# Kernel tuning notes

Hardware: AMD Instinct MI355X
Metric: run time of the kernel (lower is better)

Reference implementation:

```python
import jax, jax.numpy as jnp
import numpy as np

DIM = 1024
DIM_LATENT = 1024
DIM_HEAD = 64
INNER = max(DIM, DIM_LATENT)  # 1024
HEADS = INNER // DIM_HEAD     # 16
SCALE = DIM_HEAD ** -0.5
LN_EPS = 1e-5
RMS_EPS = 1e-8


def layernorm(x, g, b):
    mu = jnp.mean(x, axis=-1, keepdims=True)
    var = jnp.mean(jnp.square(x - mu), axis=-1, keepdims=True)
    return (x - mu) * jax.lax.rsqrt(var + LN_EPS) * g + b


def rmsnorm(x, gamma):
    # torch: x / clamp(norm(x,-1) * d**-0.5, eps) * gamma
    n = jnp.linalg.norm(x, axis=-1, keepdims=True) * (x.shape[-1] ** -0.5)
    return x / jnp.maximum(n, RMS_EPS) * gamma


def setup_inputs() -> dict:
    key = jax.random.key(0)
    ks = jax.random.split(key, 8)
    b, n, nl = 8, 2048, 512
    x = jax.random.normal(ks[0], (b, n, DIM), dtype=jnp.float32)
    latents = jax.random.normal(ks[1], (b, nl, DIM_LATENT), dtype=jnp.float32)
    mask = jax.random.randint(ks[2], (b, n), 0, 2).astype(bool)
    init = lambda k, shape, fan_in: jax.random.normal(k, shape, jnp.float32) * (fan_in ** -0.5)
    return {
        "x": x,
        "latents": latents,
        "mask": mask,
        "ln_x_g": jnp.ones((DIM,), jnp.float32),
        "ln_x_b": jnp.zeros((DIM,), jnp.float32),
        "ln_l_g": jnp.ones((DIM_LATENT,), jnp.float32),
        "ln_l_b": jnp.zeros((DIM_LATENT,), jnp.float32),
        "q_gamma": jnp.ones((DIM_HEAD,), jnp.float32),
        "k_gamma": jnp.ones((DIM_HEAD,), jnp.float32),
        "W_q": init(ks[3], (DIM_LATENT, INNER), DIM_LATENT),
        "W_kv": init(ks[4], (DIM, 2 * INNER), DIM),
        "W_out": init(ks[5], (INNER, DIM_LATENT), INNER),
        "b_out": jnp.zeros((DIM_LATENT,), jnp.float32),
    }


def reference(x, latents, mask, ln_x_g, ln_x_b, ln_l_g, ln_l_b,
              q_gamma, k_gamma, W_q, W_kv, W_out, b_out):
    b, n, _ = x.shape
    nl = latents.shape[1]
    xn = layernorm(x, ln_x_g, ln_x_b)
    ln = layernorm(latents, ln_l_g, ln_l_b)

    q = ln @ W_q                                   # [b, nl, inner]
    kv = jnp.concatenate([xn @ W_kv, ln @ W_kv], axis=1)  # [b, n+nl, 2*inner]
    k, v = kv[..., :INNER], kv[..., INNER:]

    to_heads = lambda t: t.reshape(t.shape[0], t.shape[1], HEADS, DIM_HEAD).transpose(0, 2, 1, 3)
    q, k, v = to_heads(q), to_heads(k), to_heads(v)  # [b, h, *, d]

    qn = rmsnorm(q, q_gamma) * SCALE
    kn = rmsnorm(k, k_gamma)

    sim = jnp.einsum('bhid,bhjd->bhij', qn, kn)      # [b, h, nl, n+nl]
    full_mask = jnp.pad(mask, ((0, 0), (0, nl)), constant_values=True)
    neg = -jnp.finfo(sim.dtype).max
    sim = jnp.where(full_mask[:, None, None, :], sim, neg)

    attn = jax.nn.softmax(sim.astype(jnp.float32), axis=-1).astype(sim.dtype)
    out = jnp.einsum('bhij,bhjd->bhid', attn, v)     # [b, h, nl, d]
    out = out.transpose(0, 2, 1, 3).reshape(b, nl, INNER)
    return out @ W_out + b_out
```

## Files before the change

### kernel.cpp

```cpp
#include <hip/hip_runtime.h>
#include <hip/hip_bf16.h>
#include <cfloat>
#include <cmath>

typedef __hip_bfloat16 bf16;
#define DEV_INLINE __device__ __forceinline__

typedef __attribute__((ext_vector_type(8))) short short8;
typedef __attribute__((ext_vector_type(4))) short short4v;
typedef __attribute__((ext_vector_type(4))) float float4v;
typedef __attribute__((ext_vector_type(16))) float float16v;

#define BATCH 8
#define NSEQ 2048
#define NLAT 512
#define DIM_ 1024
#define NKV 2560
#define HEADS_ 16
#define DHEAD 64
#define SCALE_ 0.125f
#define LN_EPS_ 1e-5f
#define RMS_EPS_ 1e-8f

DEV_INLINE float bf2f(bf16 v) { return __bfloat162float(v); }
DEV_INLINE bf16 f2bf(float v) { return __float2bfloat16(v); }
DEV_INLINE short bfbits(float x) { union { bf16 b; short s; } c; c.b = f2bf(x); return c.s; }
DEV_INLINE float sbits2f(short s) { union { bf16 b; short s; } c; c.s = s; return bf2f(c.b); }

DEV_INLINE int detect_bf16(const void* ones) {
    return (*(const unsigned*)ones == 0x3F803F80u) ? 1 : 0;
}

template<typename T> DEV_INLINE float ldf(const T* p);
template<> DEV_INLINE float ldf<float>(const float* p) { return *p; }
template<> DEV_INLINE float ldf<bf16>(const bf16* p)  { return __bfloat162float(*p); }

DEV_INLINE void gload16(const bf16* g, bf16* l) {
    __builtin_amdgcn_global_load_lds(
        (const __attribute__((address_space(1))) unsigned int*)g,
        (__attribute__((address_space(3))) unsigned int*)l,
        16, 0, 0);
}

DEV_INLINE float block_sum_256(float v, float* sred) {
    #pragma unroll
    for (int o = 1; o < 64; o <<= 1) v += __shfl_xor(v, o, 64);
    int w = threadIdx.x >> 6;
    __syncthreads();
    if ((threadIdx.x & 63) == 0) sred[w] = v;
    __syncthreads();
    return sred[0] + sred[1] + sred[2] + sred[3];
}

template<typename T>
DEV_INLINE void ln_row_body(int r, const void* xv, const void* latv,
                            const void* gxv, const void* bxv,
                            const void* glv, const void* blv,
                            bf16* __restrict__ out, float* sred)
{
    const T* src; const T* g; const T* be; bf16* o;
    if (r < BATCH * NSEQ) {
        int b = r >> 11, i = r & 2047;
        src = (const T*)xv + (size_t)r * DIM_;
        o = out + ((size_t)b * NKV + i) * DIM_;
        g = (const T*)gxv; be = (const T*)bxv;
    } else {
        int rr = r - BATCH * NSEQ;
        int b = rr >> 9, i = rr & 511;
        src = (const T*)latv + (size_t)rr * DIM_;
        o = out + ((size_t)b * NKV + NSEQ + i) * DIM_;
        g = (const T*)glv; be = (const T*)blv;
    }
    int t = threadIdx.x;
    float v[4];
    float s = 0.f;
    #pragma unroll
    for (int j = 0; j < 4; j++) { v[j] = ldf(src + t + j * 256); s += v[j]; }
    s = block_sum_256(s, sred);
    float mu = s * (1.f / 1024.f);
    float s2 = 0.f;
    #pragma unroll
    for (int j = 0; j < 4; j++) { float d = v[j] - mu; s2 += d * d; }
    s2 = block_sum_256(s2, sred);
    float rstd = rsqrtf(s2 * (1.f / 1024.f) + LN_EPS_);
    #pragma unroll
    for (int j = 0; j < 4; j++) {
        int c = t + j * 256;
        o[c] = f2bf((v[j] - mu) * rstd * ldf(g + c) + ldf(be + c));
    }
}

template<typename T>
DEV_INLINE void trans_body(int bid, const void* wqv, const void* wkvv, const void* woutv,
                           bf16* wqT, bf16* wkvT, bf16* woutT, float* tile )
{
    const T* in; bf16* out; int N, t0;
    if (bid < 1024)      { in = (const T*)wqv;   out = wqT;   N = 1024; t0 = bid; }
    else if (bid < 3072) { in = (const T*)wkvv;  out = wkvT;  N = 2048; t0 = bid - 1024; }
    else                 { in = (const T*)woutv; out = woutT; N = 1024; t0 = bid - 3072; }
    int K = 1024;
    int nb = N >> 5;
    int bn = (t0 % nb) * 32, bk = (t0 / nb) * 32;
    int tx = threadIdx.x & 31, ty = threadIdx.x >> 5;
    #pragma unroll
    for (int j = 0; j < 4; j++)
        tile[(ty + j * 8) * 33 + tx] = ldf(in + (size_t)(bk + ty + j * 8) * N + bn + tx);
    __syncthreads();
    #pragma unroll
    for (int j = 0; j < 4; j++)
        out[(size_t)(bn + ty + j * 8) * K + bk + tx] = f2bf(tile[tx * 33 + ty + j * 8]);
}

__global__ __launch_bounds__(256) void prep_kernel(
    const void* x, const void* lat,
    const void* gx, const void* bx, const void* gl, const void* bl,
    const void* wq, const void* wkv, const void* wout,
    bf16* __restrict__ cat_n, bf16* __restrict__ wqT,
    bf16* __restrict__ wkvT, bf16* __restrict__ woutT)
{
    __shared__ float smem[32 * 33];
    int isb = detect_bf16(gx);
    int bid = blockIdx.x;
    if (bid < 20480) {
        if (isb) ln_row_body<bf16>(bid, x, lat, gx, bx, gl, bl, cat_n, smem);
        else     ln_row_body<float>(bid, x, lat, gx, bx, gl, bl, cat_n, smem);
    } else {
        int t = bid - 20480;
        if (isb) trans_body<bf16>(t, wq, wkv, wout, wqT, wkvT, woutT, smem);
        else     trans_body<float>(t, wq, wkv, wout, wqT, wkvT, woutT, smem);
    }
}

#define MFMA_CORE_128(As, Bs, Apt, Bpt, K, acc)                                \
    {                                                                          \
        bf16* Asl_ = &As[threadIdx.x * 8];                                     \
        bf16* Bsl_ = &Bs[threadIdx.x * 8];                                     \
        for (int k0 = 0; k0 < K; k0 += 64) {                                   \
            __syncthreads();                                                   \
            _Pragma("unroll")                                                  \
            for (int rep = 0; rep < 4; rep++) {                                \
                gload16(Apt[rep] + k0, Asl_ + rep * 2048);                     \
                gload16(Bpt[rep] + k0, Bsl_ + rep * 2048);                     \
            }                                                                  \
            __syncthreads();                                                   \
            _Pragma("unroll")                                                  \
            for (int kk = 0; kk < 4; kk++) {                                   \
                short8 af_[2], bf_[2];                                         \
                _Pragma("unroll")                                              \
                for (int ms = 0; ms < 2; ms++) {                               \
                    int row = wm * 64 + ms * 32 + l32;                         \
                    int jc = (kk * 2 + h5) ^ (row & 7);                        \
                    af_[ms] = *(const short8*)&As[row * 64 + jc * 8];          \
                }                                                              \
                _Pragma("unroll")                                              \
                for (int ns = 0; ns < 2; ns++) {                               \
                    int row = wn * 64 + ns * 32 + l32;                         \
                    int jc = (kk * 2 + h5) ^ (row & 7);                        \
                    bf_[ns] = *(const short8*)&Bs[row * 64 + jc * 8];          \
                }                                                              \
                _Pragma("unroll")                                              \
                for (int ms = 0; ms < 2; ms++)                                 \
                    _Pragma("unroll")                                          \
                    for (int ns = 0; ns < 2; ns++)                             \
                        acc[ms][ns] = __builtin_amdgcn_mfma_f32_32x32x16_bf16( \
                            af_[ms], bf_[ns], acc[ms][ns], 0, 0, 0);           \
            }                                                                  \
        }                                                                      \
    }

__global__ __launch_bounds__(256) void gemm_qkv(
    const void* gq, const void* gk,
    const bf16* __restrict__ cat_n, const bf16* __restrict__ wkvT,
    const bf16* __restrict__ wqT,
    bf16* __restrict__ kbuf, bf16* __restrict__ vtbuf, bf16* __restrict__ qbuf)
{
    __shared__ bf16 As[128 * 64];
    __shared__ bf16 Bs[128 * 64];
    int isb = detect_bf16(gq);

    int tid = threadIdx.x;
    int bid = blockIdx.x;
    int wv = tid >> 6, lane = tid & 63, l32 = lane & 31, h5 = lane >> 5;
    int wm = wv >> 1, wn = wv & 1;

    const bf16* Bt; int bn, bm; bool isq;
    if (bid < 2560) {
        bm = (bid >> 7) * 8 + (bid & 7);
        bn = (bid >> 3) & 15;
        Bt = wkvT; isq = false;
    } else {
        int t = bid - 2560;
        bm = (t >> 6) * 8 + (t & 7);
        bn = (t >> 3) & 7;
        Bt = wqT; isq = true;
    }
    const int K = 1024;

    const bf16* Apt[4]; const bf16* Bpt[4];
    #pragma unroll
    for (int rep = 0; rep < 4; rep++) {
        int c = rep * 256 + tid;
        int row = c >> 3;
        int k8 = ((c & 7) ^ (row & 7)) * 8;
        int ar = bm * 128 + row;
        int am = isq ? ((ar >> 9) * NKV + NSEQ + (ar & 511)) : ar;
        Apt[rep] = cat_n + (size_t)am * K + k8;
        Bpt[rep] = Bt + (size_t)(bn * 128 + row) * K + k8;
    }

    float16v acc[2][2];
    #pragma unroll
    for (int i = 0; i < 2; i++)
        #pragma unroll
        for (int j = 0; j < 2; j++)
            #pragma unroll
            for (int r = 0; r < 16; r++) acc[i][j][r] = 0.f;

    MFMA_CORE_128(As, Bs, Apt, Bpt, K, acc);

    bool dorms = isq || (bn < 8);
    if (dorms) {
        const void* gp = isq ? gq : gk;
        float g2[2];
        #pragma unroll
        for (int ns = 0; ns < 2; ns++) {
            int idx = ns * 32 + l32;
            g2[ns] = isb ? bf2f(((const bf16*)gp)[idx]) : ((const float*)gp)[idx];
        }
        #pragma unroll
        for (int ms = 0; ms < 2; ms++) {
            #pragma unroll
            for (int reg = 0; reg < 16; reg++) {
                float ss = acc[ms][0][reg] * acc[ms][0][reg]
                         + acc[ms][1][reg] * acc[ms][1][reg];
                ss += __shfl_xor(ss, 1, 64);
                ss += __shfl_xor(ss, 2, 64);
                ss += __shfl_xor(ss, 4, 64);
                ss += __shfl_xor(ss, 8, 64);
                ss += __shfl_xor(ss, 16, 64);
                float n = sqrtf(ss) * 0.125f;
                float inv = 1.0f / fmaxf(n, RMS_EPS_);
                if (isq) inv *= SCALE_;
                acc[ms][0][reg] *= inv * g2[0];
                acc[ms][1][reg] *= inv * g2[1];
            }
        }
    }

    if (!isq && bn >= 8) {
        int bq = bm / 20;
        int keyb = (bm % 20) * 128 + wm * 64;
        #pragma unroll
        for (int ms = 0; ms < 2; ms++) {
            #pragma unroll
            for (int rg = 0; rg < 4; rg++) {
                int key = keyb + ms * 32 + rg * 8 + h5 * 4;
                #pragma unroll
                for (int ns = 0; ns < 2; ns++) {
                    int col = bn * 128 + wn * 64 + ns * 32 + l32 - 1024;
                    int h = col >> 6, d = col & 63;
                    short4v ov;
                    #pragma unroll
                    for (int rr = 0; rr < 4; rr++) ov[rr] = bfbits(acc[ms][ns][rg * 4 + rr]);
                    *(short4v*)(vtbuf + ((size_t)((bq * 16 + h) * 64 + d)) * NKV + key) = ov;
                }
            }
        }
    } else {
        bf16* C = isq ? qbuf : kbuf;
        #pragma unroll
        for (int ms = 0; ms < 2; ms++) {
            #pragma unroll
            for (int rg = 0; rg < 4; rg++) {
                int row0 = bm * 128 + wm * 64 + ms * 32 + rg * 8 + h5 * 4;
                #pragma unroll
                for (int rr = 0; rr < 4; rr++) {
                    int row = row0 + rr;
                    #pragma unroll
                    for (int ns = 0; ns < 2; ns++) {
                        int col = bn * 128 + wn * 64 + ns * 32 + l32;
                        C[(size_t)row * 1024 + col] = f2bf(acc[ms][ns][rg * 4 + rr]);
                    }
                }
            }
        }
    }
}

#define KC 64
__global__ __launch_bounds__(256) void attn_mfma(
    const bf16* __restrict__ q, const bf16* __restrict__ kbuf,
    const bf16* __restrict__ vtbuf, const int* __restrict__ maskp,
    const void* gk, bf16* __restrict__ out)
{
    __shared__ bf16 Ks[KC * 64];
    __shared__ bf16 Vt[DHEAD * 64];
    __shared__ bf16 Ps[4][2][16][64];
    __shared__ float msk_s[KC];

    int isb = detect_bf16(gk);
    int tid = threadIdx.x;
    int bid = blockIdx.x;
    int bh = bid & 127, qb = bid >> 7;
    int h = bh & 15, bb = bh >> 4;
    int wv = tid >> 6, lane = tid & 63, quad = lane >> 4, l16 = lane & 15;
    int q8 = quad * 8;
    int qbase = qb * 128 + wv * 32;
    int sw = l16 & 7;

    const bf16* kbase = kbuf + (size_t)bb * NKV * 1024 + h * DHEAD;
    const bf16* vbase = vtbuf + (size_t)(bb * 16 + h) * DHEAD * NKV;

    short8 qf[2][2];
    #pragma unroll
    for (int qt = 0; qt < 2; qt++) {
        const bf16* qp = q + ((size_t)(bb * NLAT + qbase + qt * 16 + l16)) * 1024 + h * DHEAD;
        qf[qt][0] = *(const short8*)(qp + q8);
        qf[qt][1] = *(const short8*)(qp + q8 + 32);
    }

    float gv = isb ? bf2f(((const bf16*)gk)[lane]) : ((const float*)gk)[lane];
    gv = fabsf(gv);
    #pragma unroll
    for (int o = 1; o < 64; o <<= 1) gv = fmaxf(gv, __shfl_xor(gv, o, 64));
    float m_fix[2];
    #pragma unroll
    for (int qt = 0; qt < 2; qt++) {
        float ssq = 0.f;
        #pragma unroll
        for (int j = 0; j < 8; j++) {
            float a = sbits2f(qf[qt][0][j]);
            float b = sbits2f(qf[qt][1][j]);
            ssq += a * a + b * b;
        }
        ssq += __shfl_xor(ssq, 16, 64);
        ssq += __shfl_xor(ssq, 32, 64);
        m_fix[qt] = sqrtf(ssq) * 8.0f * gv;
    }

    int c0 = tid, c1 = tid + 256;
    int krow0 = c0 >> 3, kj0 = ((c0 & 7) ^ (krow0 & 7)) * 8;
    int krow1 = c1 >> 3, kj1 = ((c1 & 7) ^ (krow1 & 7)) * 8;

    float4v o_acc[2][4];
    #pragma unroll
    for (int qt = 0; qt < 2; qt++)
        #pragma unroll
        for (int ds = 0; ds < 4; ds++)
            #pragma unroll
            for (int r = 0; r < 4; r++) o_acc[qt][ds][r] = 0.f;
    float l_i[2] = {0.f, 0.f};

    for (int kb = 0; kb < NKV; kb += KC) {
        __syncthreads();
        gload16(kbase + (size_t)(kb + krow0) * 1024 + kj0, &Ks[c0 * 8]);
        gload16(kbase + (size_t)(kb + krow1) * 1024 + kj1, &Ks[c1 * 8]);
        gload16(vbase + (size_t)krow0 * NKV + kb + kj0, &Vt[c0 * 8]);
        gload16(vbase + (size_t)krow1 * NKV + kb + kj1, &Vt[c1 * 8]);
        if (tid < KC) {
            int key = kb + tid;
            float mv = 0.f;
            if (key < NSEQ) mv = maskp[bb * NSEQ + key] ? 0.f : -1e30f;
            msk_s[tid] = mv;
        }
        __syncthreads();

        float4v st[2][4];
        #pragma unroll
        for (int kt = 0; kt < 4; kt++) {
            int row = kt * 16 + l16;
            short8 kf0 = *(const short8*)&Ks[row * 64 + ((quad ^ sw) << 3)];
            short8 kf1 = *(const short8*)&Ks[row * 64 + (((quad + 4) ^ sw) << 3)];
            #pragma unroll
            for (int qt = 0; qt < 2; qt++) {
                float4v z; z[0]=0.f; z[1]=0.f; z[2]=0.f; z[3]=0.f;
                z = __builtin_amdgcn_mfma_f32_16x16x32_bf16(kf0, qf[qt][0], z, 0, 0, 0);
                z = __builtin_amdgcn_mfma_f32_16x16x32_bf16(kf1, qf[qt][1], z, 0, 0, 0);
                st[qt][kt] = z;
            }
        }
        float4 mv4[4];
        #pragma unroll
        for (int kt = 0; kt < 4; kt++) mv4[kt] = *(const float4*)&msk_s[kt * 16 + 4 * quad];
        #pragma unroll
        for (int qt = 0; qt < 2; qt++) {
            float lp = 0.f;
            #pragma unroll
            for (int kt = 0; kt < 4; kt++) {
                const float* mk = (const float*)&mv4[kt];
                short4v pk;
                #pragma unroll
                for (int r = 0; r < 4; r++) {
                    float e = __expf(st[qt][kt][r] + mk[r] - m_fix[qt]);
                    lp += e;
                    pk[r] = bfbits(e);
                }
                int j = kt * 2 + (quad >> 1);
                int js = j ^ sw;
                *(short4v*)&Ps[wv][qt][l16][js * 8 + (quad & 1) * 4] = pk;
            }
            l_i[qt] += lp;
        }

        #pragma unroll
        for (int kc = 0; kc < 2; kc++) {
            short8 pf[2];
            #pragma unroll
            for (int qt = 0; qt < 2; qt++)
                pf[qt] = *(const short8*)&Ps[wv][qt][l16][((kc * 4 + quad) ^ sw) * 8];
            #pragma unroll
            for (int ds = 0; ds < 4; ds++) {
                int row = ds * 16 + l16;
                short8 vf = *(const short8*)&Vt[row * 64 + (((kc * 4 + quad) ^ sw) << 3)];
                #pragma unroll
                for (int qt = 0; qt < 2; qt++)
                    o_acc[qt][ds] = __builtin_amdgcn_mfma_f32_16x16x32_bf16(vf, pf[qt], o_acc[qt][ds], 0, 0, 0);
            }
        }
    }

    #pragma unroll
    for (int qt = 0; qt < 2; qt++) {
        float l = l_i[qt];
        l += __shfl_xor(l, 16, 64);
        l += __shfl_xor(l, 32, 64);
        float inv = 1.0f / l;
        bf16* op = out + ((size_t)(bb * NLAT + qbase + qt * 16 + l16)) * 1024 + h * DHEAD;
        #pragma unroll
        for (int ds = 0; ds < 4; ds++) {
            short4v ov;
            #pragma unroll
            for (int r = 0; r < 4; r++) ov[r] = bfbits(o_acc[qt][ds][r] * inv);
            *(short4v*)(op + ds * 16 + 4 * quad) = ov;
        }
    }
}

__global__ __launch_bounds__(256) void gemm_out(
    const void* ones, const void* bias,
    const bf16* __restrict__ A, const bf16* __restrict__ Bt, void* __restrict__ Cout)
{
    __shared__ bf16 As[128 * 64];
    __shared__ bf16 Bs[128 * 64];
    int isb = detect_bf16(ones);

    int tid = threadIdx.x;
    int bid = blockIdx.x;
    int bm = (bid >> 6) * 8 + (bid & 7);
    int bn = (bid >> 3) & 7;
    int wv = tid >> 6, lane = tid & 63, l32 = lane & 31, h5 = lane >> 5;
    int wm = wv >> 1, wn = wv & 1;
    const int K = 1024, N = 1024;

    const bf16* Apt[4]; const bf16* Bpt[4];
    #pragma unroll
    for (int rep = 0; rep < 4; rep++) {
        int c = rep * 256 + tid;
        int row = c >> 3;
        int k8 = ((c & 7) ^ (row & 7)) * 8;
        Apt[rep] = A + (size_t)(bm * 128 + row) * K + k8;
        Bpt[rep] = Bt + (size_t)(bn * 128 + row) * K + k8;
    }

    float16v acc[2][2];
    #pragma unroll
    for (int i = 0; i < 2; i++)
        #pragma unroll
        for (int j = 0; j < 2; j++)
            #pragma unroll
            for (int r = 0; r < 16; r++) acc[i][j][r] = 0.f;

    MFMA_CORE_128(As, Bs, Apt, Bpt, K, acc);

    #pragma unroll
    for (int ms = 0; ms < 2; ms++) {
        #pragma unroll
        for (int rg = 0; rg < 4; rg++) {
            int row0 = bm * 128 + wm * 64 + ms * 32 + rg * 8 + h5 * 4;
            #pragma unroll
            for (int rr = 0; rr < 4; rr++) {
                int row = row0 + rr;
                #pragma unroll
                for (int ns = 0; ns < 2; ns++) {
                    int col = bn * 128 + wn * 64 + ns * 32 + l32;
                    float bv = isb ? bf2f(((const bf16*)bias)[col]) : ((const float*)bias)[col];
                    float v = acc[ms][ns][rg * 4 + rr] + bv;
                    if (isb) ((bf16*)Cout)[(size_t)row * N + col] = f2bf(v);
                    else     ((float*)Cout)[(size_t)row * N + col] = v;
                }
            }
        }
    }
}

extern "C" void kernel_launch(void* const* d_in, const int* in_sizes, int n_in,
                              void* d_out, int out_size, void* d_ws, size_t ws_size,
                              hipStream_t stream) {
    const int* mask = (const int*)d_in[2];

    char* ws = (char*)d_ws;
    size_t off = 0;
    bf16* cat_n   = (bf16*)(ws + off); off += (size_t)20480 * 1024 * 2;
    bf16* kbuf    = (bf16*)(ws + off); off += (size_t)20480 * 1024 * 2;
    bf16* vtbuf   = (bf16*)(ws + off); off += (size_t)8192 * 2560 * 2;
    bf16* qbuf    = (bf16*)(ws + off); off += (size_t)4096 * 1024 * 2;
    bf16* attnout = (bf16*)(ws + off); off += (size_t)4096 * 1024 * 2;
    bf16* wqT     = (bf16*)(ws + off); off += (size_t)1024 * 1024 * 2;
    bf16* wkvT    = (bf16*)(ws + off); off += (size_t)2048 * 1024 * 2;
    bf16* woutT   = (bf16*)(ws + off); off += (size_t)1024 * 1024 * 2;

    prep_kernel<<<24576, 256, 0, stream>>>(
        d_in[0], d_in[1], d_in[3], d_in[4], d_in[5], d_in[6],
        d_in[9], d_in[10], d_in[11], cat_n, wqT, wkvT, woutT);

    gemm_qkv<<<2816, 256, 0, stream>>>(
        d_in[7], d_in[8], cat_n, wkvT, wqT, kbuf, vtbuf, qbuf);

    attn_mfma<<<512, 256, 0, stream>>>(qbuf, kbuf, vtbuf, mask, d_in[8], attnout);

    gemm_out<<<256, 256, 0, stream>>>(
        d_in[3], d_in[12], attnout, woutT, d_out);
}
```

Baseline: 391.2 us.

## Rewrite QKV GEMM with 256x256 tiles, 8 waves and pipelined direct-to-LDS loads

The QKV projection GEMM moves from 128x128 tiles on 256 threads to 256x256 tiles on 512 threads (8 waves, 2x4 layout), switching from 32x32x16 to 16x16x32 MFMA. Global loads go directly to LDS (gload16) into a multi-slot buffer with software pipelining over K halves, and explicit vmcnt waits, barriers and setprio bracket the MFMA clusters. The RMSnorm and V-transpose epilogues are rewritten for the new accumulator layout. The aim is higher arithmetic intensity and overlap of memory with compute, at the cost of higher register pressure and a large LDS footprint (128KB per block).

```diff
diff --git a/kernel.cpp b/kernel.cpp
--- a/kernel.cpp
+++ b/kernel.cpp
@@ -168,120 +168,175 @@
         }                                                                      \
     }
 
-__global__ __launch_bounds__(256) void gemm_qkv(
+#define QKV_MFMA(NB)                                                          \
+    __builtin_amdgcn_s_barrier(); asm volatile("" ::: "memory");              \
+    __builtin_amdgcn_s_setprio(1);                                            \
+    _Pragma("unroll")                                                         \
+    for (int m_ = 0; m_ < 8; m_++) {                                          \
+        acc[m_][NB] = __builtin_amdgcn_mfma_f32_16x16x32_bf16(                \
+            af[m_], bq[0], acc[m_][NB], 0, 0, 0);                             \
+        acc[m_][NB + 1] = __builtin_amdgcn_mfma_f32_16x16x32_bf16(            \
+            af[m_], bq[1], acc[m_][NB + 1], 0, 0, 0);                         \
+    }                                                                         \
+    __builtin_amdgcn_s_setprio(0);                                            \
+    __builtin_amdgcn_s_barrier(); asm volatile("" ::: "memory");
+
+__global__ __launch_bounds__(512, 2) void gemm_qkv(
     const void* gq, const void* gk,
     const bf16* __restrict__ cat_n, const bf16* __restrict__ wkvT,
     const bf16* __restrict__ wqT,
     bf16* __restrict__ kbuf, bf16* __restrict__ vtbuf, bf16* __restrict__ qbuf)
 {
-    __shared__ bf16 As[128 * 64];
-    __shared__ bf16 Bs[128 * 64];
+    __shared__ bf16 S[8][8192];
     int isb = detect_bf16(gq);
-
     int tid = threadIdx.x;
     int bid = blockIdx.x;
-    int wv = tid >> 6, lane = tid & 63, l32 = lane & 31, h5 = lane >> 5;
-    int wm = wv >> 1, wn = wv & 1;
-
-    const bf16* Bt; int bn, bm; bool isq;
-    if (bid < 2560) {
-        bm = (bid >> 7) * 8 + (bid & 7);
-        bn = (bid >> 3) & 15;
-        Bt = wkvT; isq = false;
-    } else {
-        int t = bid - 2560;
-        bm = (t >> 6) * 8 + (t & 7);
-        bn = (t >> 3) & 7;
-        Bt = wqT; isq = true;
-    }
-    const int K = 1024;
-
-    const bf16* Apt[4]; const bf16* Bpt[4];
-    #pragma unroll
-    for (int rep = 0; rep < 4; rep++) {
-        int c = rep * 256 + tid;
-        int row = c >> 3;
-        int k8 = ((c & 7) ^ (row & 7)) * 8;
-        int ar = bm * 128 + row;
-        int am = isq ? ((ar >> 9) * NKV + NSEQ + (ar & 511)) : ar;
-        Apt[rep] = cat_n + (size_t)am * K + k8;
-        Bpt[rep] = Bt + (size_t)(bn * 128 + row) * K + k8;
-    }
-
-    float16v acc[2][2];
-    #pragma unroll
-    for (int i = 0; i < 2; i++)
-        #pragma unroll
-        for (int j = 0; j < 2; j++)
-            #pragma unroll
-            for (int r = 0; r < 16; r++) acc[i][j][r] = 0.f;
-
-    MFMA_CORE_128(As, Bs, Apt, Bpt, K, acc);
-
-    bool dorms = isq || (bn < 8);
-    if (dorms) {
+    int lane = tid & 63;
+    int l16 = lane & 15, quad = lane >> 4;
+    int wv = tid >> 6;
+    int wm = wv >> 2, wn = wv & 3;
+
+    int x = bid & 7, ii = bid >> 3;
+    int bm, bn; bool isq; const bf16* Bt;
+    if (ii < 80) { bm = (ii >> 3) * 8 + x; bn = ii & 7; Bt = wkvT; isq = false; }
+    else { int j = ii - 80; bm = (j >> 2) * 8 + x; bn = j & 3; Bt = wqT; isq = true; }
+
+    int r0 = tid >> 2;
+    int c0 = (tid & 3) ^ (r0 & 3);
+    int r1 = (tid + 512) >> 2;
+    int c1 = (tid & 3) ^ (r1 & 3);
+    int ar0 = bm * 256 + r0, ar1 = bm * 256 + r1;
+    size_t ga0 = isq ? ((size_t)(ar0 >> 9) * NKV + NSEQ + (ar0 & 511)) : (size_t)ar0;
+    size_t ga1 = isq ? ((size_t)(ar1 >> 9) * NKV + NSEQ + (ar1 & 511)) : (size_t)ar1;
+    const bf16* pA0 = cat_n + ga0 * 1024 + c0 * 8;
+    const bf16* pA1 = cat_n + ga1 * 1024 + c1 * 8;
+    const bf16* pB0 = Bt + (size_t)(bn * 256 + r0) * 1024 + c0 * 8;
+    const bf16* pB1 = Bt + (size_t)(bn * 256 + r1) * 1024 + c1 * 8;
+
+#define STG(P0, P1, SLOT, KO) do {                                            \
+        gload16((P0) + (KO), &S[SLOT][0] + tid * 8);                          \
+        gload16((P1) + (KO), &S[SLOT][0] + 4096 + tid * 8);                   \
+    } while (0)
+
+    int qx = (quad ^ (l16 & 3)) * 8;
+    int aoff = (wm * 128 + l16) * 32 + qx;
+    int boff = (wn * 64 + l16) * 32 + qx;
+
+    float4v acc[8][4];
+    #pragma unroll
+    for (int m = 0; m < 8; m++)
+        #pragma unroll
+        for (int n = 0; n < 4; n++)
+            #pragma unroll
+            for (int r = 0; r < 4; r++) acc[m][n][r] = 0.f;
+
+    STG(pA0, pA1, 0, 0);
+    STG(pB0, pB1, 2, 0);
+    STG(pA0, pA1, 1, 32);
+    STG(pB0, pB1, 3, 32);
+    STG(pA0, pA1, 4, 64);
+    STG(pB0, pB1, 6, 64);
+    asm volatile("s_waitcnt vmcnt(4)" ::: "memory");
+    __builtin_amdgcn_s_barrier(); asm volatile("" ::: "memory");
+
+    short8 af[8], bq[2];
+    for (int t = 0; t < 16; ++t) {
+        int cur = (t & 1) * 4, nxt = cur ^ 4;
+        const bf16* A0k = &S[cur + 0][0];
+        const bf16* A1k = &S[cur + 1][0];
+        const bf16* B0k = &S[cur + 2][0];
+        const bf16* B1k = &S[cur + 3][0];
+        int ko1 = t * 64 + 96;
+        int ko2 = t * 64 + 128;
+
+        #pragma unroll
+        for (int m = 0; m < 8; m++) af[m] = *(const short8*)&A0k[aoff + m * 512];
+        bq[0] = *(const short8*)&B0k[boff];
+        bq[1] = *(const short8*)&B0k[boff + 512];
+        if (t < 15) STG(pA0, pA1, nxt + 1, ko1);
+        QKV_MFMA(0)
+
+        bq[0] = *(const short8*)&B0k[boff + 1024];
+        bq[1] = *(const short8*)&B0k[boff + 1536];
+        if (t < 15) STG(pB0, pB1, nxt + 3, ko1);
+        QKV_MFMA(2)
+
+        #pragma unroll
+        for (int m = 0; m < 8; m++) af[m] = *(const short8*)&A1k[aoff + m * 512];
+        bq[0] = *(const short8*)&B1k[boff];
+        bq[1] = *(const short8*)&B1k[boff + 512];
+        if (t < 14) STG(pA0, pA1, cur + 0, ko2);
+        QKV_MFMA(0)
+
+        bq[0] = *(const short8*)&B1k[boff + 1024];
+        bq[1] = *(const short8*)&B1k[boff + 1536];
+        if (t < 14) {
+            STG(pB0, pB1, cur + 2, ko2);
+            asm volatile("s_waitcnt vmcnt(4)" ::: "memory");
+        } else {
+            asm volatile("s_waitcnt vmcnt(0)" ::: "memory");
+        }
+        QKV_MFMA(2)
+    }
+#undef STG
+
+    if (isq || bn < 4) {
         const void* gp = isq ? gq : gk;
-        float g2[2];
-        #pragma unroll
-        for (int ns = 0; ns < 2; ns++) {
-            int idx = ns * 32 + l32;
-            g2[ns] = isb ? bf2f(((const bf16*)gp)[idx]) : ((const float*)gp)[idx];
-        }
-        #pragma unroll
-        for (int ms = 0; ms < 2; ms++) {
-            #pragma unroll
-            for (int reg = 0; reg < 16; reg++) {
-                float ss = acc[ms][0][reg] * acc[ms][0][reg]
-                         + acc[ms][1][reg] * acc[ms][1][reg];
+        float g2[4];
+        #pragma unroll
+        for (int n = 0; n < 4; n++) {
+            int idx = n * 16 + l16;
+            g2[n] = isb ? bf2f(((const bf16*)gp)[idx]) : ((const float*)gp)[idx];
+        }
+        #pragma unroll
+        for (int m = 0; m < 8; m++) {
+            #pragma unroll
+            for (int r = 0; r < 4; r++) {
+                float ss = acc[m][0][r] * acc[m][0][r]
+                         + acc[m][1][r] * acc[m][1][r]
+                         + acc[m][2][r] * acc[m][2][r]
+                         + acc[m][3][r] * acc[m][3][r];
                 ss += __shfl_xor(ss, 1, 64);
                 ss += __shfl_xor(ss, 2, 64);
                 ss += __shfl_xor(ss, 4, 64);
                 ss += __shfl_xor(ss, 8, 64);
-                ss += __shfl_xor(ss, 16, 64);
-                float n = sqrtf(ss) * 0.125f;
-                float inv = 1.0f / fmaxf(n, RMS_EPS_);
+                float nn = sqrtf(ss) * 0.125f;
+                float inv = 1.0f / fmaxf(nn, RMS_EPS_);
                 if (isq) inv *= SCALE_;
-                acc[ms][0][reg] *= inv * g2[0];
-                acc[ms][1][reg] *= inv * g2[1];
-            }
-        }
-    }
-
-    if (!isq && bn >= 8) {
-        int bq = bm / 20;
-        int keyb = (bm % 20) * 128 + wm * 64;
-        #pragma unroll
-        for (int ms = 0; ms < 2; ms++) {
-            #pragma unroll
-            for (int rg = 0; rg < 4; rg++) {
-                int key = keyb + ms * 32 + rg * 8 + h5 * 4;
                 #pragma unroll
-                for (int ns = 0; ns < 2; ns++) {
-                    int col = bn * 128 + wn * 64 + ns * 32 + l32 - 1024;
-                    int h = col >> 6, d = col & 63;
-                    short4v ov;
-                    #pragma unroll
-                    for (int rr = 0; rr < 4; rr++) ov[rr] = bfbits(acc[ms][ns][rg * 4 + rr]);
-                    *(short4v*)(vtbuf + ((size_t)((bq * 16 + h) * 64 + d)) * NKV + key) = ov;
-                }
+                for (int n = 0; n < 4; n++) acc[m][n][r] *= inv * g2[n];
+            }
+        }
+    }
+
+    if (!isq && bn >= 4) {
+        int bq_ = bm / 10;
+        int key0 = (bm % 10) * 256 + wm * 128;
+        #pragma unroll
+        for (int m = 0; m < 8; m++) {
+            int key = key0 + m * 16 + quad * 4;
+            #pragma unroll
+            for (int n = 0; n < 4; n++) {
+                int col = bn * 256 + wn * 64 + n * 16 + l16 - 1024;
+                int h = col >> 6, d = col & 63;
+                short4v ov;
+                #pragma unroll
+                for (int r = 0; r < 4; r++) ov[r] = bfbits(acc[m][n][r]);
+                *(short4v*)(vtbuf + ((size_t)((bq_ * 16 + h) * 64 + d)) * NKV + key) = ov;
             }
         }
     } else {
         bf16* C = isq ? qbuf : kbuf;
-        #pragma unroll
-        for (int ms = 0; ms < 2; ms++) {
-            #pragma unroll
-            for (int rg = 0; rg < 4; rg++) {
-                int row0 = bm * 128 + wm * 64 + ms * 32 + rg * 8 + h5 * 4;
+        int rbase = bm * 256 + wm * 128;
+        int cbase = bn * 256 + wn * 64;
+        #pragma unroll
+        for (int m = 0; m < 8; m++) {
+            #pragma unroll
+            for (int r = 0; r < 4; r++) {
+                int row = rbase + m * 16 + quad * 4 + r;
                 #pragma unroll
-                for (int rr = 0; rr < 4; rr++) {
-                    int row = row0 + rr;
-                    #pragma unroll
-                    for (int ns = 0; ns < 2; ns++) {
-                        int col = bn * 128 + wn * 64 + ns * 32 + l32;
-                        C[(size_t)row * 1024 + col] = f2bf(acc[ms][ns][rg * 4 + rr]);
-                    }
-                }
+                for (int n = 0; n < 4; n++)
+                    C[(size_t)row * 1024 + cbase + n * 16 + l16] = f2bf(acc[m][n][r]);
             }
         }
     }
@@ -513,7 +568,7 @@
         d_in[0], d_in[1], d_in[3], d_in[4], d_in[5], d_in[6],
         d_in[9], d_in[10], d_in[11], cat_n, wqT, wkvT, woutT);
 
-    gemm_qkv<<<2816, 256, 0, stream>>>(
+    gemm_qkv<<<704, 512, 0, stream>>>(
         d_in[7], d_in[8], cat_n, wkvT, wqT, kbuf, vtbuf, qbuf);
 
     attn_mfma<<<512, 256, 0, stream>>>(qbuf, kbuf, vtbuf, mask, d_in[8], attnout);
```

Result: faster. 362.0 us (-7.4%).
